# Kernel optimization log

Hardware: AMD Instinct MI355X
Metric: run time of the kernel (lower is better)

Reference implementation:

```python
import jax, jax.numpy as jnp
import numpy as np


def _conv1d(x, w, b, stride=1, pad=0):
    # x: [B, Cin, L], w: [Cout, Cin, K] (torch OIH layout)
    y = jax.lax.conv_general_dilated(
        x, w, window_strides=(stride,), padding=[(pad, pad)],
        dimension_numbers=('NCH', 'OIH', 'NCH'))
    return y + b[None, :, None]


def setup_inputs() -> dict:
    key = jax.random.key(0)
    ks = jax.random.split(key, 8)
    B, M, C, Hf, Wf, Ho, Wo = 4, 112, 512, 13, 13, 16, 16
    return {
        'features_f': jax.random.normal(ks[0], (B, C, Hf, Wf), jnp.float32),   # cfp last feature map
        'oct_feats':  jax.random.normal(ks[1], (B, M, C, Ho, Wo), jnp.float32),  # per-slice last feature maps
        'conv1d_w':   jax.random.normal(ks[2], (64, 1024, 64), jnp.float32) * 0.02,
        'conv1d_b':   jnp.zeros((64,), jnp.float32),
        'convf_w':    jax.random.normal(ks[3], (13, 64, 5), jnp.float32) * 0.05,
        'convf_b':    jnp.zeros((13,), jnp.float32),
        'head_w':     jax.random.normal(ks[4], (3, 1536), jnp.float32) * 0.02,
        'head_b':     jnp.zeros((3,), jnp.float32),
    }


def reference(features_f, oct_feats, conv1d_w, conv1d_b, convf_w, convf_b, head_w, head_b):
    B, M, C, Ho, Wo = oct_feats.shape
    # per-slice global avg / max pools of encoder_o feature maps -> [B, M, C]
    fv = oct_feats.mean(axis=(3, 4))
    fv_max = oct_feats.max(axis=(3, 4))
    # slice attention: conv1d over slice axis on concatenated [B, 2C, M]
    x = jnp.concatenate([fv, fv_max], axis=2).transpose(0, 2, 1)
    slice_weights = jax.nn.sigmoid(_conv1d(x, conv1d_w, conv1d_b))  # [B, 64, M-63]
    # argmax-indexed per-channel gather: for each (b, c) pick the slice whose
    # pooled activation is largest, then copy that slice's [Ho, Wo] map.
    idx = jnp.argmax(fv, axis=1)          # [B, C]
    idx_max = jnp.argmax(fv_max, axis=1)  # [B, C]
    sel = jnp.take_along_axis(oct_feats, idx[:, None, :, None, None], axis=1)[:, 0]        # [B, C, Ho, Wo]
    sel_max = jnp.take_along_axis(oct_feats, idx_max[:, None, :, None, None], axis=1)[:, 0]
    feat_o_avg = sel.mean(axis=(2, 3))      # original applies avgpool to both selections
    feat_o_max = sel_max.mean(axis=(2, 3))
    feat_o = jnp.concatenate([feat_o_avg, feat_o_max], axis=1)  # [B, 1024]
    # fundus attention map r: [B, 13, 13], broadcast over C channels
    r = jax.nn.sigmoid(_conv1d(slice_weights, convf_w, convf_b, stride=4, pad=2))
    attended = features_f + r[:, None, :, :] * features_f
    feat_f = attended.mean(axis=(2, 3))     # [B, 512]
    feat = jnp.concatenate([feat_f, feat_o], axis=1)  # [B, 1536]
    # classification head (dropout is identity at inference): Linear(1536 -> 3)
    return feat @ head_w.T + head_b
```

## Files before the change

kernel.cpp:

```cpp
#include <hip/hip_runtime.h>
#include <hip/hip_bf16.h>
#include <math.h>

#define XB_OFF  0
#define FO_OFF  917504
#define AM_OFF  933888
#define SW_OFF  933888
#define FVX_OFF 984064
#define FVA_OFF 1901568
#define SPILL_NEED (FVA_OFF + 917504)

__global__ __launch_bounds__(256) void k_pool1(const float* __restrict__ oct,
                                               __hip_bfloat16* __restrict__ xb,
                                               float* __restrict__ fvx,
                                               float* __restrict__ fva) {
    int wg = (blockIdx.x * 256 + threadIdx.x) >> 6;
    int lane = threadIdx.x & 63;
    const float4* p = (const float4*)(oct + (size_t)wg * 256);
    float4 v = p[lane];
    float s  = v.x + v.y + v.z + v.w;
    float mx = fmaxf(fmaxf(v.x, v.y), fmaxf(v.z, v.w));
#pragma unroll
    for (int off = 32; off >= 1; off >>= 1) {
        s  += __shfl_xor(s, off);
        mx  = fmaxf(mx, __shfl_xor(mx, off));
    }
    if (lane == 0) {
        int c  = wg & 511;
        int bm = wg >> 9;
        int m  = bm % 112;
        int b  = bm / 112;
        float fv = s * (1.0f / 256.0f);
        xb[((size_t)b * 1024 + c) * 112 + m]       = __float2bfloat16(fv);
        xb[((size_t)b * 1024 + 512 + c) * 112 + m] = __float2bfloat16(mx);
        fvx[((size_t)b * 512 + c) * 112 + m] = mx;
        fva[((size_t)b * 512 + c) * 112 + m] = fv;
    }
}

__global__ __launch_bounds__(256) void k_pool2(const float* __restrict__ fvx,
                                               const float* __restrict__ fva,
                                               float* __restrict__ fo) {
    int wid  = blockIdx.x * 4 + (threadIdx.x >> 6);
    int lane = threadIdx.x & 63;
    int b = wid >> 9, c = wid & 511;
    const float* kx = fvx + (size_t)wid * 112;
    const float* va = fva + (size_t)wid * 112;
    int m0 = lane, m1 = lane + 64;
    float k0 = (m0 < 112) ? kx[m0] : -INFINITY;
    float k1 = (m1 < 112) ? kx[m1] : -INFINITY;
    float f0 = (m0 < 112) ? va[m0] : -INFINITY;
    float f1 = (m1 < 112) ? va[m1] : -INFINITY;
    float bk; int bm;
    if (k1 > k0) { bk = k1; bm = m1; } else { bk = k0; bm = m0; }
    float bf = fmaxf(f0, f1);
#pragma unroll
    for (int off = 32; off >= 1; off >>= 1) {
        float ok = __shfl_xor(bk, off);
        int   om = __shfl_xor(bm, off);
        if (ok > bk || (ok == bk && om < bm)) { bk = ok; bm = om; }
        bf = fmaxf(bf, __shfl_xor(bf, off));
    }
    if (lane == 0) {
        fo[b * 1024 + c]       = bf;
        fo[b * 1024 + 512 + c] = va[bm];
    }
}

__global__ __launch_bounds__(256) void k_init(unsigned long long* __restrict__ am) {
    am[blockIdx.x * 256 + threadIdx.x] = 0ULL;
}

__global__ __launch_bounds__(256) void k_pool(const float* __restrict__ oct,
                                              __hip_bfloat16* __restrict__ xb,
                                              unsigned long long* __restrict__ am) {
    int wg = (blockIdx.x * 256 + threadIdx.x) >> 6;
    int lane = threadIdx.x & 63;
    const float4* p = (const float4*)(oct + (size_t)wg * 256);
    float4 v = p[lane];
    float s  = v.x + v.y + v.z + v.w;
    float mx = fmaxf(fmaxf(v.x, v.y), fmaxf(v.z, v.w));
#pragma unroll
    for (int off = 32; off >= 1; off >>= 1) {
        s  += __shfl_xor(s, off);
        mx  = fmaxf(mx, __shfl_xor(mx, off));
    }
    if (lane == 0) {
        int c  = wg & 511;
        int bm = wg >> 9;
        int m  = bm % 112;
        int b  = bm / 112;
        xb[((size_t)b * 1024 + c) * 112 + m]       = __float2bfloat16(s * (1.0f / 256.0f));
        xb[((size_t)b * 1024 + 512 + c) * 112 + m] = __float2bfloat16(mx);
        unsigned int u = __float_as_uint(mx);
        unsigned int key = (u & 0x80000000u) ? ~u : (u | 0x80000000u);
        unsigned long long pk = ((unsigned long long)key << 32) | (unsigned int)(111 - m);
        atomicMax(&am[b * 512 + c], pk);
    }
}

__global__ __launch_bounds__(256) void k_feato(const __hip_bfloat16* __restrict__ xb,
                                               const unsigned long long* __restrict__ am,
                                               float* __restrict__ fo) {
    int wid  = blockIdx.x * 4 + (threadIdx.x >> 6);
    int lane = threadIdx.x & 63;
    int b = wid >> 9, c = wid & 511;
    const __hip_bfloat16* fvrow = xb + ((size_t)b * 1024 + c) * 112;
    float v0 = (lane < 112)      ? __bfloat162float(fvrow[lane])      : -INFINITY;
    float v1 = (lane + 64 < 112) ? __bfloat162float(fvrow[lane + 64]) : -INFINITY;
    float mxf = fmaxf(v0, v1);
#pragma unroll
    for (int off = 32; off >= 1; off >>= 1)
        mxf = fmaxf(mxf, __shfl_xor(mxf, off));
    if (lane == 0) {
        int mstar = 111 - (int)(unsigned int)(am[b * 512 + c] & 0xFFFFFFFFULL);
        fo[b * 1024 + c]       = mxf;
        fo[b * 1024 + 512 + c] = __bfloat162float(fvrow[mstar]);
    }
}

__global__ __launch_bounds__(256) void k_conv(const __hip_bfloat16* __restrict__ xb,
                                              const float* __restrict__ w1,
                                              const float* __restrict__ b1,
                                              float* __restrict__ sw) {
    __shared__ unsigned int xs[256 * 61];
    __shared__ float red[4][25];
    int bx = blockIdx.x;
    int lh = bx & 1, co = (bx >> 1) & 63, b = bx >> 7;
    int t = threadIdx.x, wv = t >> 6, lane = t & 63;
    int l0u = lh * 12;
    float acc[25];
#pragma unroll
    for (int i = 0; i < 25; i++) acc[i] = 0.f;
    const unsigned int* gxb = (const unsigned int*)xb;
    for (int chunk = 0; chunk < 4; chunk++) {
        __syncthreads();
        for (int r = wv; r < 256; r += 4)
            if (lane < 56)
                xs[r * 61 + lane] = gxb[((size_t)b * 1024 + chunk * 256 + r) * 56 + lane];
        __syncthreads();
        int cil = wv * 64 + lane;
        int ci  = chunk * 256 + cil;
        const unsigned int* xu = xs + cil * 61 + l0u;
        float xf[88];
#pragma unroll
        for (int i = 0; i < 44; i++) {
            unsigned int u = xu[i];
            xf[2 * i]     = __uint_as_float(u << 16);
            xf[2 * i + 1] = __uint_as_float(u & 0xffff0000u);
        }
        const float* wrow = w1 + ((size_t)co * 1024 + ci) * 64;
#pragma unroll
        for (int kc = 0; kc < 4; kc++) {
            float ww[16];
#pragma unroll
            for (int j = 0; j < 16; j++) ww[j] = wrow[kc * 16 + j];
#pragma unroll
            for (int k = 0; k < 16; k++)
#pragma unroll
                for (int i = 0; i < 25; i++)
                    acc[i] += ww[k] * xf[kc * 16 + k + i];
        }
    }
#pragma unroll
    for (int i = 0; i < 25; i++) {
#pragma unroll
        for (int off = 32; off >= 1; off >>= 1)
            acc[i] += __shfl_xor(acc[i], off);
    }
    if (lane < 25) red[wv][lane] = acc[lane];
    __syncthreads();
    if (t < 25) {
        float s = red[0][t] + red[1][t] + red[2][t] + red[3][t] + b1[co];
        float sg = 1.f / (1.f + expf(-s));
        int l = lh * 24 + t;
        if (!(lh == 1 && t == 0))
            sw[(size_t)(b * 64 + co) * 49 + l] = sg;
    }
}

__global__ __launch_bounds__(256) void k_tail(const float* __restrict__ sw,
                                              const float* __restrict__ cw,
                                              const float* __restrict__ cb,
                                              const float* __restrict__ ff,
                                              const float* __restrict__ fo,
                                              const float* __restrict__ hw,
                                              const float* __restrict__ hb,
                                              float* __restrict__ out) {
    __shared__ float swl[3136];
    __shared__ float cwl[4160];
    __shared__ float rfl[169];
    __shared__ float ffl[512];
    __shared__ float hred[3][4];
    int b = blockIdx.x, t = threadIdx.x, w = t >> 6, lane = t & 63;
    for (int i = t; i < 3136; i += 256) swl[i] = sw[b * 3136 + i];
    for (int i = t; i < 4160; i += 256) cwl[i] = cw[i];
    __syncthreads();
    if (t < 169) {
        int o = t / 13, l = t % 13;
        float s = cb[o];
        for (int i = 0; i < 64; i++) {
#pragma unroll
            for (int k = 0; k < 5; k++) {
                int pos = 4 * l + k - 2;
                if (pos >= 0 && pos < 49)
                    s += swl[i * 49 + pos] * cwl[(o * 64 + i) * 5 + k];
            }
        }
        rfl[t] = 1.f + 1.f / (1.f + expf(-s));
    }
    __syncthreads();
    {
        float acc1 = 0.f, acc2 = 0.f;
        const float* r1 = ff + ((size_t)b * 512 + t) * 169;
        const float* r2 = r1 + 256 * 169;
        for (int pidx = 0; pidx < 169; ++pidx) {
            float rv = rfl[pidx];
            acc1 += r1[pidx] * rv;
            acc2 += r2[pidx] * rv;
        }
        ffl[t]       = acc1 * (1.0f / 169.0f);
        ffl[t + 256] = acc2 * (1.0f / 169.0f);
    }
    __syncthreads();
    {
        float s0 = 0.f, s1 = 0.f, s2 = 0.f;
#pragma unroll
        for (int rep = 0; rep < 6; ++rep) {
            int i = rep * 256 + t;
            float fv = (i < 512) ? ffl[i] : fo[b * 1024 + (i - 512)];
            s0 += fv * hw[i];
            s1 += fv * hw[1536 + i];
            s2 += fv * hw[3072 + i];
        }
#pragma unroll
        for (int off = 32; off >= 1; off >>= 1) {
            s0 += __shfl_xor(s0, off);
            s1 += __shfl_xor(s1, off);
            s2 += __shfl_xor(s2, off);
        }
        if (lane == 0) { hred[0][w] = s0; hred[1][w] = s1; hred[2][w] = s2; }
    }
    __syncthreads();
    if (t < 3)
        out[b * 3 + t] = hred[t][0] + hred[t][1] + hred[t][2] + hred[t][3] + hb[t];
}

extern "C" void kernel_launch(void* const* d_in, const int* in_sizes, int n_in,
                              void* d_out, int out_size, void* d_ws, size_t ws_size,
                              hipStream_t stream) {
    const float* ff  = (const float*)d_in[0];
    const float* oct = (const float*)d_in[1];
    const float* w1  = (const float*)d_in[2];
    const float* b1  = (const float*)d_in[3];
    const float* cw  = (const float*)d_in[4];
    const float* cb  = (const float*)d_in[5];
    const float* hw  = (const float*)d_in[6];
    const float* hb  = (const float*)d_in[7];
    float* out = (float*)d_out;
    char* ws = (char*)d_ws;
    __hip_bfloat16*     xb = (__hip_bfloat16*)(ws + XB_OFF);
    float*              fo = (float*)(ws + FO_OFF);
    unsigned long long* am = (unsigned long long*)(ws + AM_OFF);
    float*              sw = (float*)(ws + SW_OFF);

    if (ws_size >= (size_t)SPILL_NEED) {
        float* fvx = (float*)(ws + FVX_OFF);
        float* fva = (float*)(ws + FVA_OFF);
        hipLaunchKernelGGL(k_pool1, dim3(57344), dim3(256), 0, stream, oct, xb, fvx, fva);
        hipLaunchKernelGGL(k_pool2, dim3(512),   dim3(256), 0, stream, fvx, fva, fo);
    } else {
        hipLaunchKernelGGL(k_init,  dim3(8),     dim3(256), 0, stream, am);
        hipLaunchKernelGGL(k_pool,  dim3(57344), dim3(256), 0, stream, oct, xb, am);
        hipLaunchKernelGGL(k_feato, dim3(512),   dim3(256), 0, stream, xb, am, fo);
    }
    hipLaunchKernelGGL(k_conv, dim3(512), dim3(256), 0, stream, xb, w1, b1, sw);
    hipLaunchKernelGGL(k_tail, dim3(4),   dim3(256), 0, stream, sw, cw, cb, ff, fo, hw, hb, out);
}
```

Before: 466.6 us.

## Write pooled stats as contiguous float2 and transpose to bf16 in second pass

The pooling kernel now writes one float2 (max, mean) per (b,m,c) in natural order, so consecutive waves produce contiguous stores. Before, each wave did four scattered strided stores into transposed bf16 and float arrays. The bf16 transpose into the conv input layout moves to the second kernel, which stages a row per wave in shared memory and writes coalesced 32-bit words. The selected mean value is also carried through the argmax shuffle, which removes a dependent gather load. In exchange the second kernel gains strided float2 reads across m and a block barrier.

```diff
diff --git a/kernel.cpp b/kernel.cpp
--- a/kernel.cpp
+++ b/kernel.cpp
@@ -6,14 +6,11 @@
 #define FO_OFF  917504
 #define AM_OFF  933888
 #define SW_OFF  933888
-#define FVX_OFF 984064
-#define FVA_OFF 1901568
-#define SPILL_NEED (FVA_OFF + 917504)
+#define FVP_OFF 984064
+#define SPILL_NEED (FVP_OFF + 1835008)
 
 __global__ __launch_bounds__(256) void k_pool1(const float* __restrict__ oct,
-                                               __hip_bfloat16* __restrict__ xb,
-                                               float* __restrict__ fvx,
-                                               float* __restrict__ fva) {
+                                               float2* __restrict__ fvp) {
     int wg = (blockIdx.x * 256 + threadIdx.x) >> 6;
     int lane = threadIdx.x & 63;
     const float4* p = (const float4*)(oct + (size_t)wg * 256);
@@ -25,45 +22,54 @@
         s  += __shfl_xor(s, off);
         mx  = fmaxf(mx, __shfl_xor(mx, off));
     }
-    if (lane == 0) {
-        int c  = wg & 511;
-        int bm = wg >> 9;
-        int m  = bm % 112;
-        int b  = bm / 112;
-        float fv = s * (1.0f / 256.0f);
-        xb[((size_t)b * 1024 + c) * 112 + m]       = __float2bfloat16(fv);
-        xb[((size_t)b * 1024 + 512 + c) * 112 + m] = __float2bfloat16(mx);
-        fvx[((size_t)b * 512 + c) * 112 + m] = mx;
-        fva[((size_t)b * 512 + c) * 112 + m] = fv;
-    }
-}
-
-__global__ __launch_bounds__(256) void k_pool2(const float* __restrict__ fvx,
-                                               const float* __restrict__ fva,
+    if (lane == 0)
+        fvp[wg] = make_float2(mx, s * (1.0f / 256.0f));
+}
+
+__global__ __launch_bounds__(256) void k_pool2(const float2* __restrict__ fvp,
+                                               __hip_bfloat16* __restrict__ xb,
                                                float* __restrict__ fo) {
-    int wid  = blockIdx.x * 4 + (threadIdx.x >> 6);
-    int lane = threadIdx.x & 63;
+    __shared__ unsigned int sfv[4][56];
+    __shared__ unsigned int smx[4][56];
+    int t = threadIdx.x, w = t >> 6, lane = t & 63;
+    int wid = blockIdx.x * 4 + w;
     int b = wid >> 9, c = wid & 511;
-    const float* kx = fvx + (size_t)wid * 112;
-    const float* va = fva + (size_t)wid * 112;
-    int m0 = lane, m1 = lane + 64;
-    float k0 = (m0 < 112) ? kx[m0] : -INFINITY;
-    float k1 = (m1 < 112) ? kx[m1] : -INFINITY;
-    float f0 = (m0 < 112) ? va[m0] : -INFINITY;
-    float f1 = (m1 < 112) ? va[m1] : -INFINITY;
-    float bk; int bm;
-    if (k1 > k0) { bk = k1; bm = m1; } else { bk = k0; bm = m0; }
+    __hip_bfloat16* fvrow = (__hip_bfloat16*)sfv[w];
+    __hip_bfloat16* mxrow = (__hip_bfloat16*)smx[w];
+    float2 v0 = fvp[((size_t)b * 112 + lane) * 512 + c];
+    float k0 = v0.x, f0 = v0.y;
+    fvrow[lane] = __float2bfloat16(f0);
+    mxrow[lane] = __float2bfloat16(k0);
+    float k1 = -INFINITY, f1 = -INFINITY;
+    if (lane < 48) {
+        float2 v1 = fvp[((size_t)b * 112 + lane + 64) * 512 + c];
+        k1 = v1.x; f1 = v1.y;
+        fvrow[lane + 64] = __float2bfloat16(f1);
+        mxrow[lane + 64] = __float2bfloat16(k1);
+    }
+    float bk, bp; int bm;
+    if (k1 > k0) { bk = k1; bm = lane + 64; bp = f1; }
+    else         { bk = k0; bm = lane;      bp = f0; }
     float bf = fmaxf(f0, f1);
 #pragma unroll
     for (int off = 32; off >= 1; off >>= 1) {
         float ok = __shfl_xor(bk, off);
         int   om = __shfl_xor(bm, off);
-        if (ok > bk || (ok == bk && om < bm)) { bk = ok; bm = om; }
+        float op = __shfl_xor(bp, off);
+        if (ok > bk || (ok == bk && om < bm)) { bk = ok; bm = om; bp = op; }
         bf = fmaxf(bf, __shfl_xor(bf, off));
     }
     if (lane == 0) {
         fo[b * 1024 + c]       = bf;
-        fo[b * 1024 + 512 + c] = va[bm];
+        fo[b * 1024 + 512 + c] = bp;
+    }
+    __syncthreads();
+    int cbase = (blockIdx.x * 4) & 511;
+    unsigned int* xo = (unsigned int*)xb;
+    if (t < 224) {
+        int row = t / 56, col = t % 56;
+        xo[((size_t)b * 1024 + cbase + row) * 56 + col]       = sfv[row][col];
+        xo[((size_t)b * 1024 + 512 + cbase + row) * 56 + col] = smx[row][col];
     }
 }
 
@@ -265,10 +271,9 @@
     float*              sw = (float*)(ws + SW_OFF);
 
     if (ws_size >= (size_t)SPILL_NEED) {
-        float* fvx = (float*)(ws + FVX_OFF);
-        float* fva = (float*)(ws + FVA_OFF);
-        hipLaunchKernelGGL(k_pool1, dim3(57344), dim3(256), 0, stream, oct, xb, fvx, fva);
-        hipLaunchKernelGGL(k_pool2, dim3(512),   dim3(256), 0, stream, fvx, fva, fo);
+        float2* fvp = (float2*)(ws + FVP_OFF);
+        hipLaunchKernelGGL(k_pool1, dim3(57344), dim3(256), 0, stream, oct, fvp);
+        hipLaunchKernelGGL(k_pool2, dim3(512),   dim3(256), 0, stream, fvp, xb, fo);
     } else {
         hipLaunchKernelGGL(k_init,  dim3(8),     dim3(256), 0, stream, am);
         hipLaunchKernelGGL(k_pool,  dim3(57344), dim3(256), 0, stream, oct, xb, am);
```

New measurement: 470.7 us. No clear change (+0.9%).
